# Performance work log

Hardware: AMD Instinct MI355X
Metric: run time of the kernel (lower is better)

## Reference

```python
import jax, jax.numpy as jnp
import numpy as np

ND, NL, E, M = 8000, 16000, 60000, 50000  # disease nodes, lncrna nodes, edges, label edges
H = 16  # attention heads


def _gat(h_src, h_dst, src, dst, Ws, Wd, a_s, a_d, b, n_dst):
    # PyG GATConv: bipartite, concat heads, add_self_loops=False, negative_slope=0.2
    Hh, C = a_s.shape
    zs = (h_src @ Ws).reshape(-1, Hh, C)   # [Ns,H,C]
    zd = (h_dst @ Wd).reshape(-1, Hh, C)   # [Nd,H,C]
    al = (zs * a_s).sum(-1)[src] + (zd * a_d).sum(-1)[dst]  # [E,H]
    al = jax.nn.leaky_relu(al, negative_slope=0.2)
    m = jax.ops.segment_max(al, dst, num_segments=n_dst)
    m = jnp.where(jnp.isfinite(m), m, 0.0)  # guard empty segments
    e = jnp.exp(al - m[dst])
    s = jax.ops.segment_sum(e, dst, num_segments=n_dst)
    alpha = e / (s[dst] + 1e-16)            # softmax over incoming edges per dst
    msg = zs[src] * alpha[:, :, None]       # [E,H,C]
    out = jax.ops.segment_sum(msg, dst, num_segments=n_dst)
    return out.reshape(n_dst, Hh * C) + b


def _head_mean(x):
    x = jax.nn.relu(x)
    return x.reshape(x.shape[0], H, -1).mean(axis=1)


def _forward(x_d, x_l, emb_d, emb_l, lin_dw, lin_db, lin_lw, lin_lb,
             Wsrc1, Wdst1, asrc1, adst1, b1,
             Wsrc2, Wdst2, asrc2, adst2, b2,
             Wsrc3, Wdst3, asrc3, adst3, b3,
             pw, pb, fc1w, fc1b, fc2w, fc2b,
             node_id_d, node_id_l, edge_src, edge_dst, label_src, label_dst):
    hd = x_d @ lin_dw + lin_db + emb_d[node_id_d]   # [ND,128]
    hl = x_l @ lin_lw + lin_lb + emb_l[node_id_l]   # [NL,128]
    for (Ws, Wd, a_s, a_d, b) in ((Wsrc1, Wdst1, asrc1, adst1, b1),
                                  (Wsrc2, Wdst2, asrc2, adst2, b2),
                                  (Wsrc3, Wdst3, asrc3, adst3, b3)):
        # to_hetero: edge-type 0 = disease->lncrna (target lncrna); 1 = reverse
        out_l = _gat(hd, hl, edge_src, edge_dst, Ws[0], Wd[0], a_s[0], a_d[0], b[0], NL)
        out_d = _gat(hl, hd, edge_dst, edge_src, Ws[1], Wd[1], a_s[1], a_d[1], b[1], ND)
        hd, hl = _head_mean(out_d), _head_mean(out_l)
    # penalty scaling (per node type after to_hetero); transformer branch is dead code
    hd = hd * jnp.exp(hd @ pw[0] + pb[0])
    hl = hl * jnp.exp(hl @ pw[1] + pb[1])
    f = jnp.concatenate([hd[label_src], hl[label_dst]], axis=-1)  # [M,64]
    return jax.nn.relu(f @ fc1w + fc1b) @ fc2w + fc2b              # [M,1]


def setup_inputs():
    key = jax.random.key(0)
    ks = jax.random.split(key, 40)
    def rn(i, shape, scale=1.0):
        return jax.random.normal(ks[i], shape, dtype=jnp.float32) * scale
    return dict(
        x_d=rn(0, (ND, 412)), x_l=rn(1, (NL, 240)),
        node_id_d=jnp.arange(ND), node_id_l=jnp.arange(NL),
        edge_src=jax.random.randint(ks[2], (E,), 0, ND),
        edge_dst=jax.random.randint(ks[3], (E,), 0, NL),
        label_src=jax.random.randint(ks[4], (M,), 0, ND),
        label_dst=jax.random.randint(ks[5], (M,), 0, NL),
        emb_d=rn(6, (ND, 128), 0.1), emb_l=rn(7, (NL, 128), 0.1),
        lin_dw=rn(8, (412, 128), 412 ** -0.5), lin_db=rn(9, (128,), 0.02),
        lin_lw=rn(10, (240, 128), 240 ** -0.5), lin_lb=rn(11, (128,), 0.02),
        Wsrc1=rn(12, (2, 128, 2048), 128 ** -0.5), Wdst1=rn(13, (2, 128, 2048), 128 ** -0.5),
        asrc1=rn(14, (2, H, 128), 0.05), adst1=rn(15, (2, H, 128), 0.05), b1=rn(16, (2, 2048), 0.02),
        Wsrc2=rn(17, (2, 128, 2048), 128 ** -0.5), Wdst2=rn(18, (2, 128, 2048), 128 ** -0.5),
        asrc2=rn(19, (2, H, 128), 0.05), adst2=rn(20, (2, H, 128), 0.05), b2=rn(21, (2, 2048), 0.02),
        Wsrc3=rn(22, (2, 128, 512), 128 ** -0.5), Wdst3=rn(23, (2, 128, 512), 128 ** -0.5),
        asrc3=rn(24, (2, H, 32), 0.05), adst3=rn(25, (2, H, 32), 0.05), b3=rn(26, (2, 512), 0.02),
        pw=rn(27, (2, 32, 1), 0.05), pb=rn(28, (2, 1), 0.01),
        fc1w=rn(29, (64, 64), 64 ** -0.5), fc1b=rn(30, (64,), 0.02),
        fc2w=rn(31, (64, 1), 64 ** -0.5), fc2b=rn(32, (1,), 0.02),
    )


def reference(x_d, x_l, node_id_d, node_id_l, edge_src, edge_dst, label_src, label_dst,
              emb_d, emb_l, lin_dw, lin_db, lin_lw, lin_lb,
              Wsrc1, Wdst1, asrc1, adst1, b1,
              Wsrc2, Wdst2, asrc2, adst2, b2,
              Wsrc3, Wdst3, asrc3, adst3, b3,
              pw, pb, fc1w, fc1b, fc2w, fc2b):
    return _forward(x_d, x_l, emb_d, emb_l, lin_dw, lin_db, lin_lw, lin_lb,
                    Wsrc1, Wdst1, asrc1, adst1, b1,
                    Wsrc2, Wdst2, asrc2, adst2, b2,
                    Wsrc3, Wdst3, asrc3, adst3, b3,
                    pw, pb, fc1w, fc1b, fc2w, fc2b,
                    node_id_d, node_id_l, edge_src, edge_dst, label_src, label_dst)
```

## Files before the change

kernel.cpp:

```cpp
#include <hip/hip_runtime.h>
#include <cstdint>
#include <cstddef>

#define ND 8000
#define NL 16000
#define NE 60000
#define NM 50000

#define BM 64
#define BN 64
#define BK 16

typedef __attribute__((ext_vector_type(8))) short bf16x8;
typedef __attribute__((ext_vector_type(4))) float f32x4;
typedef __attribute__((ext_vector_type(8))) unsigned int u32x8;

__device__ __forceinline__ unsigned short f2bf(float x) {
    unsigned int u = __float_as_uint(x);
    unsigned int r = (u + 0x7FFFu + ((u >> 16) & 1u)) >> 16;
    return (unsigned short)r;
}
__device__ __forceinline__ float bf2f(unsigned short b) {
    return __uint_as_float(((unsigned int)b) << 16);
}
__device__ __forceinline__ float lrelu(float x) {
    return x >= 0.f ? x : 0.2f * x;
}

__global__ __launch_bounds__(256) void gemm3_kernel(
    const float* __restrict__ hd, const float* __restrict__ hl,
    const float* __restrict__ W,
    float* __restrict__ zs3d, float* __restrict__ zs3l)
{
    __shared__ float As[BK][BM + 4];
    __shared__ float Bs[BK][BN + 4];
    int mt = blockIdx.y;
    const float* A; const float* B; float* Cm;
    if (mt < 125) { A = hd; B = W; Cm = zs3d; }
    else { mt -= 125; A = hl; B = W + 128 * 512; Cm = zs3l; }
    const int tid = threadIdx.x;
    const int tx = tid & 15, ty = tid >> 4;
    const int bm = mt * BM, bn = blockIdx.x * BN;
    float acc[4][4] = {};
    for (int k0 = 0; k0 < 128; k0 += BK) {
#pragma unroll
        for (int i = 0; i < 4; ++i) {
            int idx = tid + i * 256;
            int ml = idx >> 4, kl = idx & 15;
            As[kl][ml] = A[(size_t)(bm + ml) * 128 + k0 + kl];
        }
#pragma unroll
        for (int i = 0; i < 4; ++i) {
            int idx = tid + i * 256;
            int kl = idx >> 6, nl = idx & 63;
            Bs[kl][nl] = B[(size_t)(k0 + kl) * 512 + bn + nl];
        }
        __syncthreads();
#pragma unroll
        for (int k = 0; k < BK; ++k) {
            float4 av = *(const float4*)&As[k][ty * 4];
            float4 bv = *(const float4*)&Bs[k][tx * 4];
            float a4[4] = {av.x, av.y, av.z, av.w};
            float b4[4] = {bv.x, bv.y, bv.z, bv.w};
#pragma unroll
            for (int i = 0; i < 4; ++i)
#pragma unroll
                for (int j = 0; j < 4; ++j)
                    acc[i][j] += a4[i] * b4[j];
        }
        __syncthreads();
    }
#pragma unroll
    for (int i = 0; i < 4; ++i) {
        int gm = bm + ty * 4 + i;
        int gn0 = bn + tx * 4;
        float4 v;
        float* vp = &v.x;
#pragma unroll
        for (int j = 0; j < 4; ++j) vp[j] = acc[i][j];
        *(float4*)&Cm[(size_t)gm * 512 + gn0] = v;
    }
}

__global__ __launch_bounds__(256) void inlin_kernel(
    const float* __restrict__ x_d, const float* __restrict__ x_l,
    const float* __restrict__ wd, const float* __restrict__ wl,
    const float* __restrict__ bd, const float* __restrict__ bl,
    const float* __restrict__ embd, const float* __restrict__ embl,
    const int* __restrict__ nidd, const int* __restrict__ nidl,
    float* __restrict__ hd, float* __restrict__ hl)
{
    __shared__ float As[BK][32 + 4];
    __shared__ float Bs[BK][BN + 4];
    int mt = blockIdx.y;
    const float* A; const float* B; const float* bias; const float* emb;
    const int* nid; float* out;
    int K;
    if (mt < 250) {
        A = x_d; B = wd; bias = bd; emb = embd; nid = nidd; out = hd; K = 412;
    } else {
        mt -= 250;
        A = x_l; B = wl; bias = bl; emb = embl; nid = nidl; out = hl; K = 240;
    }
    const int tid = threadIdx.x;
    const int tx = tid & 15, ty = tid >> 4;
    const int bm = mt * 32, bn = blockIdx.x * BN;

    const int aml0 = tid >> 4, akl0 = tid & 15;
    const int aml1 = (tid + 256) >> 4, akl1 = tid & 15;
    const int bkl = tid >> 6, bnl = tid & 63;

    float pa[2], pb[4];
    {
        int gk0 = akl0, gk1 = akl1;
        pa[0] = (gk0 < K) ? A[(size_t)(bm + aml0) * K + gk0] : 0.f;
        pa[1] = (gk1 < K) ? A[(size_t)(bm + aml1) * K + gk1] : 0.f;
#pragma unroll
        for (int i = 0; i < 4; ++i) {
            int gk = bkl + i * 4;
            pb[i] = (gk < K) ? B[(size_t)gk * 128 + bn + bnl] : 0.f;
        }
    }

    float acc[2][4] = {};
    for (int k0 = 0; k0 < K; k0 += BK) {
        As[akl0][aml0] = pa[0];
        As[akl1][aml1] = pa[1];
#pragma unroll
        for (int i = 0; i < 4; ++i)
            Bs[bkl + i * 4][bnl] = pb[i];
        __syncthreads();
        int kn = k0 + BK;
        if (kn < K) {
            int gk0 = kn + akl0, gk1 = kn + akl1;
            pa[0] = (gk0 < K) ? A[(size_t)(bm + aml0) * K + gk0] : 0.f;
            pa[1] = (gk1 < K) ? A[(size_t)(bm + aml1) * K + gk1] : 0.f;
#pragma unroll
            for (int i = 0; i < 4; ++i) {
                int gk = kn + bkl + i * 4;
                pb[i] = (gk < K) ? B[(size_t)gk * 128 + bn + bnl] : 0.f;
            }
        }
#pragma unroll
        for (int k = 0; k < BK; ++k) {
            float a0 = As[k][ty * 2];
            float a1 = As[k][ty * 2 + 1];
            float4 bv = *(const float4*)&Bs[k][tx * 4];
            float b4[4] = {bv.x, bv.y, bv.z, bv.w};
#pragma unroll
            for (int j = 0; j < 4; ++j) {
                acc[0][j] += a0 * b4[j];
                acc[1][j] += a1 * b4[j];
            }
        }
        __syncthreads();
    }
#pragma unroll
    for (int i = 0; i < 2; ++i) {
        int gm = bm + ty * 2 + i;
        int gn0 = bn + tx * 4;
        const float* ep = emb + (size_t)nid[gm] * 128 + gn0;
        float4 v;
        float* vp = &v.x;
#pragma unroll
        for (int j = 0; j < 4; ++j)
            vp[j] = acc[i][j] + bias[gn0 + j] + ep[j];
        *(float4*)&out[(size_t)gm * 128 + gn0] = v;
    }
}

__global__ void wt2_kernel(const float* __restrict__ W0, const float* __restrict__ W1,
                           unsigned short* __restrict__ WtH, unsigned short* __restrict__ WtL)
{
    int gid = blockIdx.x * 256 + threadIdx.x;
    if (gid >= 2 * 2 * 128 * 2048) return;
    int l = gid >> 19;
    int rem0 = gid & 524287;
    int dir = rem0 >> 18;
    int rem = rem0 & 262143;
    int k = rem >> 11, n = rem & 2047;
    const float* W = l ? W1 : W0;
    float v = W[(size_t)dir * 262144 + (size_t)k * 2048 + n];
    unsigned short hb = f2bf(v);
    unsigned short lb = f2bf(v - bf2f(hb));
    int u = n >> 4;
    int lane = (n & 15) + 16 * ((k >> 3) & 3);
    size_t o = (size_t)l * 524288 + (size_t)dir * 262144 +
               ((size_t)u * 4 + (k >> 5)) * 512 + lane * 8 + (k & 7);
    WtH[o] = hb;
    WtL[o] = lb;
}

__global__ __launch_bounds__(256) void gemm2r_kernel(
    const unsigned int* __restrict__ haggP,
    const unsigned short* __restrict__ WtH, const unsigned short* __restrict__ WtL,
    const float* __restrict__ bias, float* __restrict__ out, int M)
{
    const int wave = threadIdx.x >> 6;
    const int lane = threadIdx.x & 63;
    const int i = blockIdx.x;
    const int cb = (i >> 3) & 3;
    const int mt = (i >> 5) * 8 + (i & 7);
    if (mt >= (M >> 6)) return;
    const int m0 = mt * 64 + wave * 16;
    const int t = m0 >> 4;
    const int row = lane & 15;
    const int quad = lane >> 4;

    f32x4 mean[2] = {};

    u32x8 pA[4];
#pragma unroll
    for (int kc = 0; kc < 4; ++kc)
        pA[kc] = *(const u32x8*)(haggP + (((size_t)t * 16 + 0) * 4 + kc) * 512 + lane * 8);

    for (int h = 0; h < 16; ++h) {
        bf16x8 aH[4], aL[4];
#pragma unroll
        for (int kc = 0; kc < 4; ++kc) {
#pragma unroll
            for (int ii = 0; ii < 8; ++ii) {
                aH[kc][ii] = (short)(pA[kc][ii] & 0xffffu);
                aL[kc][ii] = (short)(pA[kc][ii] >> 16);
            }
        }
        if (h < 15) {
#pragma unroll
            for (int kc = 0; kc < 4; ++kc)
                pA[kc] = *(const u32x8*)(haggP + (((size_t)t * 16 + h + 1) * 4 + kc) * 512 + lane * 8);
        }

        f32x4 accH[2], accL[2];
#pragma unroll
        for (int ctl = 0; ctl < 2; ++ctl) {
            float bv = bias[h * 128 + cb * 32 + ctl * 16 + row];
            accH[ctl] = (f32x4){bv, bv, bv, bv};
            accL[ctl] = (f32x4){0.f, 0.f, 0.f, 0.f};
        }
#pragma unroll
        for (int kc = 0; kc < 4; ++kc) {
#pragma unroll
            for (int ctl = 0; ctl < 2; ++ctl) {
                const int u = h * 8 + cb * 2 + ctl;
                const size_t boff = ((size_t)u * 4 + kc) * 512 + lane * 8;
                bf16x8 bH = *(const bf16x8*)(WtH + boff);
                bf16x8 bL = *(const bf16x8*)(WtL + boff);
                accH[ctl] = __builtin_amdgcn_mfma_f32_16x16x32_bf16(aH[kc], bH, accH[ctl], 0, 0, 0);
                accL[ctl] = __builtin_amdgcn_mfma_f32_16x16x32_bf16(aH[kc], bL, accL[ctl], 0, 0, 0);
                accL[ctl] = __builtin_amdgcn_mfma_f32_16x16x32_bf16(aL[kc], bH, accL[ctl], 0, 0, 0);
            }
        }
#pragma unroll
        for (int ctl = 0; ctl < 2; ++ctl)
#pragma unroll
            for (int r = 0; r < 4; ++r)
                mean[ctl][r] += fmaxf(accH[ctl][r] + accL[ctl][r], 0.f);
    }

#pragma unroll
    for (int ctl = 0; ctl < 2; ++ctl) {
        int c = cb * 32 + ctl * 16 + row;
#pragma unroll
        for (int r = 0; r < 4; ++r) {
            int gm = m0 + quad * 4 + r;
            out[(size_t)gm * 128 + c] = mean[ctl][r] * (1.f / 16.f);
        }
    }
}

__global__ void fold3_kernel(
    const float* __restrict__ Ws1, const float* __restrict__ Wd1,
    const float* __restrict__ as1, const float* __restrict__ ad1,
    const float* __restrict__ Ws2, const float* __restrict__ Wd2,
    const float* __restrict__ as2, const float* __restrict__ ad2,
    const float* __restrict__ Ws3, const float* __restrict__ Wd3,
    const float* __restrict__ as3, const float* __restrict__ ad3,
    float* __restrict__ fw3)
{
    int gid = blockIdx.x * blockDim.x + threadIdx.x;
    if (gid >= 3 * 4 * 128 * 16) return;
    int l = gid / 8192, rem1 = gid % 8192;
    int f = rem1 / 2048, rem = rem1 % 2048;
    int k = rem >> 4, h = rem & 15;
    int Ntot = (l == 2) ? 512 : 2048;
    int C = Ntot >> 4;
    const float* W;
    const float* a;
    if (l == 0) { W = (f & 1) ? Wd1 : Ws1; a = (f & 1) ? ad1 : as1; }
    else if (l == 1) { W = (f & 1) ? Wd2 : Ws2; a = (f & 1) ? ad2 : as2; }
    else { W = (f & 1) ? Wd3 : Ws3; a = (f & 1) ? ad3 : as3; }
    if (f >= 2) { W += 128 * Ntot; a += 16 * C; }
    float s = 0.f;
    for (int c = 0; c < C; ++c) s += W[(size_t)k * Ntot + h * C + c] * a[h * C + c];
    fw3[gid] = s;
}

__global__ __launch_bounds__(256) void score2both_kernel(
    const float* __restrict__ Hd, const float* __restrict__ Hl,
    const float* __restrict__ fw,
    float* __restrict__ ssb0, float* __restrict__ sdb1,
    float* __restrict__ sdb0, float* __restrict__ ssb1)
{
    __shared__ float hs[16 * 128];
    __shared__ float wa[128 * 16];
    __shared__ float wb[128 * 16];
    int b = blockIdx.x;
    const float* Hf; const float* WfA; const float* WfB;
    float* outA; float* outB; int n0;
    if (b < ND / 16) {
        Hf = Hd; WfA = fw; WfB = fw + 3 * 2048; outA = ssb0; outB = sdb1; n0 = b * 16;
    } else {
        Hf = Hl; WfA = fw + 1 * 2048; WfB = fw + 2 * 2048; outA = sdb0; outB = ssb1;
        n0 = (b - ND / 16) * 16;
    }
    int tid = threadIdx.x;
#pragma unroll
    for (int i = 0; i < 8; ++i) {
        int idx = tid + i * 256;
        int nl = idx >> 7, k = idx & 127;
        hs[idx] = Hf[(size_t)(n0 + nl) * 128 + k];
        wa[idx] = WfA[idx];
        wb[idx] = WfB[idx];
    }
    __syncthreads();
    int nl = tid >> 4, h = tid & 15;
    float sa = 0.f, sb = 0.f;
    for (int k = 0; k < 128; ++k) {
        float hv = hs[nl * 128 + k];
        sa += hv * wa[k * 16 + h];
        sb += hv * wb[k * 16 + h];
    }
    int gn = n0 + nl;
    outA[gn * 16 + h] = sa;
    outB[gn * 16 + h] = sb;
}

__global__ void ms_kernel(
    const int* __restrict__ esrc, const int* __restrict__ edst,
    const float* __restrict__ ssb0, const float* __restrict__ sdb0,
    const float* __restrict__ ssb1, const float* __restrict__ sdb1,
    const int* __restrict__ offl, const int* __restrict__ csrl, float* __restrict__ msl,
    const int* __restrict__ offd, const int* __restrict__ csrd, float* __restrict__ msd)
{
    int t = blockIdx.x * 256 + threadIdx.x;
    const int* off; const int* csr; const int* srcidx;
    const float* ss; float sdv; float* ms; int d, h;
    if (t < NL * 16) {
        d = t >> 4; h = t & 15;
        off = offl; csr = csrl; srcidx = esrc; ss = ssb0;
        sdv = sdb0[d * 16 + h]; ms = msl;
    } else {
        t -= NL * 16;
        if (t >= ND * 16) return;
        d = t >> 4; h = t & 15;
        off = offd; csr = csrd; srcidx = edst; ss = ssb1;
        sdv = sdb1[d * 16 + h]; ms = msd;
    }
    int e0 = off[d], e1 = off[d + 1];
    float m = -1e30f, s = 0.f;
    for (int e = e0; e < e1; ++e) {
        int sn = srcidx[csr[e]];
        float a = lrelu(ss[sn * 16 + h] + sdv);
        if (a > m) { s = s * __expf(m - a) + 1.f; m = a; }
        else s += __expf(a - m);
    }
    ms[d * 32 + h] = m;
    ms[d * 32 + 16 + h] = s + 1e-16f;
}

__global__ void hist_kernel(const int* __restrict__ esrc, const int* __restrict__ edst,
                            int* __restrict__ degl, int* __restrict__ degd)
{
    int e = blockIdx.x * blockDim.x + threadIdx.x;
    if (e >= NE) return;
    atomicAdd(&degl[edst[e]], 1);
    atomicAdd(&degd[esrc[e]], 1);
}

__global__ __launch_bounds__(1024) void scan2_kernel(
    const int* __restrict__ degA, int* __restrict__ offA, int nA,
    const int* __restrict__ degB, int* __restrict__ offB, int nB)
{
    __shared__ int ps[1024];
    const int* deg = blockIdx.x ? degB : degA;
    int* off = blockIdx.x ? offB : offA;
    int n = blockIdx.x ? nB : nA;
    int tid = threadIdx.x;
    int chunk = (n + 1023) >> 10;
    int start = tid * chunk, end = min(start + chunk, n);
    int p = 0;
    for (int i = start; i < end; ++i) p += deg[i];
    ps[tid] = p;
    __syncthreads();
    for (int o = 1; o < 1024; o <<= 1) {
        int v = (tid >= o) ? ps[tid - o] : 0;
        __syncthreads();
        ps[tid] += v;
        __syncthreads();
    }
    int run = ps[tid] - p;
    for (int i = start; i < end; ++i) { off[i] = run; run += deg[i]; }
    if (tid == 1023) off[n] = ps[1023];
}

__global__ void scatter_kernel(const int* __restrict__ esrc, const int* __restrict__ edst,
                               const int* __restrict__ offl, const int* __restrict__ offd,
                               int* __restrict__ curl, int* __restrict__ curd,
                               int* __restrict__ csrl, int* __restrict__ csrd)
{
    int e = blockIdx.x * blockDim.x + threadIdx.x;
    if (e >= NE) return;
    int dl = edst[e]; int p = atomicAdd(&curl[dl], 1); csrl[offl[dl] + p] = e;
    int dd = esrc[e]; int q = atomicAdd(&curd[dd], 1); csrd[offd[dd] + q] = e;
}

__global__ __launch_bounds__(256) void hagg_kernel(
    const float* __restrict__ hsrc,
    const float* __restrict__ ss,
    const float* __restrict__ sd,
    const float* __restrict__ ms,
    const int* __restrict__ off, const int* __restrict__ csr, const int* __restrict__ srcidx,
    unsigned int* __restrict__ haggP)
{
    __shared__ float alpha_s[2][8][17];
    __shared__ int src_s[2][8];
    const int d0 = blockIdx.x * 2;
    const int tid = threadIdx.x;

    const int half = tid >> 7;
    const int c = tid & 127;
    const int d = d0 + half;
    const int my_e0 = off[d];
    const int my_deg = off[d + 1] - my_e0;
    const int deg0 = off[d0 + 1] - off[d0];
    const int deg1 = off[d0 + 2] - off[d0 + 1];
    const int degmax = deg0 > deg1 ? deg0 : deg1;
    const int ntrip = (degmax + 7) >> 3;

    float acc[16];
#pragma unroll
    for (int h = 0; h < 16; ++h) acc[h] = 0.f;

    for (int trip = 0; trip < ntrip; ++trip) {
        int ce = trip * 8;
        {
            int ei = c >> 4, h = c & 15;
            if (ce + ei < my_deg) {
                int eid = csr[my_e0 + ce + ei];
                int sn = srcidx[eid];
                float a = lrelu(ss[sn * 16 + h] + sd[d * 16 + h]);
                alpha_s[half][ei][h] = __expf(a - ms[d * 32 + h]) / ms[d * 32 + 16 + h];
                if (h == 0) src_s[half][ei] = sn;
            }
        }
        __syncthreads();
        int nc = min(8, my_deg - ce);
        for (int ei = 0; ei < nc; ++ei) {
            float v = hsrc[(size_t)src_s[half][ei] * 128 + c];
#pragma unroll
            for (int h = 0; h < 16; ++h)
                acc[h] += alpha_s[half][ei][h] * v;
        }
        __syncthreads();
    }

    const int t = d >> 4;
    const int lane8 = ((d & 15) + 16 * ((c >> 3) & 3)) * 8 + (c & 7);
    const int kc = c >> 5;
#pragma unroll
    for (int h = 0; h < 16; ++h) {
        float v = acc[h];
        unsigned short hb = f2bf(v);
        unsigned short lb = f2bf(v - bf2f(hb));
        size_t idx = (((size_t)t * 16 + h) * 4 + kc) * 512 + lane8;
        haggP[idx] = (unsigned int)hb | ((unsigned int)lb << 16);
    }
}

__global__ __launch_bounds__(256) void agg32both_kernel(
    const float* __restrict__ zs3d, const float* __restrict__ zs3l,
    const float* __restrict__ ssb0, const float* __restrict__ sdb0, const float* __restrict__ msl,
    const float* __restrict__ ssb1, const float* __restrict__ sdb1, const float* __restrict__ msd,
    const int* __restrict__ offl, const int* __restrict__ csrl,
    const int* __restrict__ offd, const int* __restrict__ csrd,
    const int* __restrict__ esrc, const int* __restrict__ edst,
    const float* __restrict__ bias512,
    const float* __restrict__ pw, const float* __restrict__ pb,
    float* __restrict__ hlp, float* __restrict__ hdp)
{
    __shared__ float alpha_s[16][17];
    __shared__ int src_s[16];
    __shared__ float lds_out[512];
    __shared__ float hrow[32];
    int d = blockIdx.x;
    const float* zs; const float* ss; const float* sd; const float* ms;
    const int* off; const int* csr; const int* srcidx;
    const float* bias; const float* pwt; const float* pbt; float* out;
    if (d < NL) {
        zs = zs3d; ss = ssb0; sd = sdb0; ms = msl;
        off = offl; csr = csrl; srcidx = esrc;
        bias = bias512; pwt = pw + 32; pbt = pb + 1; out = hlp;
    } else {
        d -= NL;
        zs = zs3l; ss = ssb1; sd = sdb1; ms = msd;
        off = offd; csr = csrd; srcidx = edst;
        bias = bias512 + 512; pwt = pw; pbt = pb; out = hdp;
    }
    const int tid = threadIdx.x;
    const int e0 = off[d], e1 = off[d + 1];

    float acc0 = 0.f, acc1 = 0.f;
    const int hsel = tid >> 4;

    for (int ce = e0; ce < e1; ce += 16) {
        int nc = min(16, e1 - ce);
        if (tid < nc * 16) {
            int ei = tid >> 4, h = tid & 15;
            int eid = csr[ce + ei];
            int sn = srcidx[eid];
            float a = lrelu(ss[sn * 16 + h] + sd[d * 16 + h]);
            alpha_s[ei][h] = __expf(a - ms[d * 32 + h]) / ms[d * 32 + 16 + h];
            if (h == 0) src_s[ei] = sn;
        }
        __syncthreads();
        for (int ei = 0; ei < nc; ++ei) {
            float a = alpha_s[ei][hsel];
            float2 v = *(const float2*)(zs + (size_t)src_s[ei] * 512 + tid * 2);
            acc0 += a * v.x;
            acc1 += a * v.y;
        }
        __syncthreads();
    }

    lds_out[tid * 2] = fmaxf(acc0 + bias[tid * 2], 0.f);
    lds_out[tid * 2 + 1] = fmaxf(acc1 + bias[tid * 2 + 1], 0.f);
    __syncthreads();
    if (tid < 32) {
        float s = 0.f;
#pragma unroll
        for (int hh = 0; hh < 16; ++hh) s += lds_out[hh * 32 + tid];
        hrow[tid] = s * (1.f / 16.f);
    }
    __syncthreads();
    if (tid < 32) {
        float t = pbt[0];
#pragma unroll
        for (int c = 0; c < 32; ++c) t += hrow[c] * pwt[c];
        out[(size_t)d * 32 + tid] = hrow[tid] * expf(t);
    }
}

__global__ __launch_bounds__(256) void mlp_kernel(
    const float* __restrict__ hd, const float* __restrict__ hl,
    const int* __restrict__ ls, const int* __restrict__ ld,
    const float* __restrict__ w1, const float* __restrict__ b1,
    const float* __restrict__ w2, const float* __restrict__ b2,
    float* __restrict__ out, int M)
{
    __shared__ float w1s[64 * 64];
    __shared__ float b1s[64];
    __shared__ float w2s[64];
    int tid = threadIdx.x;
#pragma unroll
    for (int i = 0; i < 16; ++i) w1s[tid + i * 256] = w1[tid + i * 256];
    if (tid < 64) { b1s[tid] = b1[tid]; w2s[tid] = w2[tid]; }
    __syncthreads();
    int m = blockIdx.x * 256 + tid;
    if (m >= M) return;
    float f[64];
    const float* hp = hd + (size_t)ls[m] * 32;
    const float* lp = hl + (size_t)ld[m] * 32;
#pragma unroll
    for (int c = 0; c < 32; ++c) { f[c] = hp[c]; f[32 + c] = lp[c]; }
    float o = b2[0];
    for (int j = 0; j < 64; ++j) {
        float hj = b1s[j];
#pragma unroll
        for (int k = 0; k < 64; ++k) hj += f[k] * w1s[k * 64 + j];
        hj = fmaxf(hj, 0.f);
        o += hj * w2s[j];
    }
    out[m] = o;
}

extern "C" void kernel_launch(void* const* d_in, const int* in_sizes, int n_in,
                              void* d_out, int out_size, void* d_ws, size_t ws_size,
                              hipStream_t stream)
{
    const float* x_d = (const float*)d_in[0];
    const float* x_l = (const float*)d_in[1];
    const int* node_id_d = (const int*)d_in[2];
    const int* node_id_l = (const int*)d_in[3];
    const int* edge_src = (const int*)d_in[4];
    const int* edge_dst = (const int*)d_in[5];
    const int* label_src = (const int*)d_in[6];
    const int* label_dst = (const int*)d_in[7];
    const float* emb_d = (const float*)d_in[8];
    const float* emb_l = (const float*)d_in[9];
    const float* lin_dw = (const float*)d_in[10];
    const float* lin_db = (const float*)d_in[11];
    const float* lin_lw = (const float*)d_in[12];
    const float* lin_lb = (const float*)d_in[13];
    const float* Ws[3] = {(const float*)d_in[14], (const float*)d_in[19], (const float*)d_in[24]};
    const float* Wd[3] = {(const float*)d_in[15], (const float*)d_in[20], (const float*)d_in[25]};
    const float* as_[3] = {(const float*)d_in[16], (const float*)d_in[21], (const float*)d_in[26]};
    const float* ad_[3] = {(const float*)d_in[17], (const float*)d_in[22], (const float*)d_in[27]};
    const float* bb[3] = {(const float*)d_in[18], (const float*)d_in[23], (const float*)d_in[28]};
    const float* pw = (const float*)d_in[29];
    const float* pb = (const float*)d_in[30];
    const float* fc1w = (const float*)d_in[31];
    const float* fc1b = (const float*)d_in[32];
    const float* fc2w = (const float*)d_in[33];
    const float* fc2b = (const float*)d_in[34];

    char* wsb = (char*)d_ws;
    size_t woff = 0;
    auto carve = [&](size_t bytes) -> void* {
        woff = (woff + 255) & ~(size_t)255;
        void* p = wsb + woff;
        woff += bytes;
        return p;
    };
    float* hdA = (float*)carve((size_t)ND * 128 * 4);
    float* hlA = (float*)carve((size_t)NL * 128 * 4);
    float* hdB = (float*)carve((size_t)ND * 128 * 4);
    float* hlB = (float*)carve((size_t)NL * 128 * 4);
    unsigned int* haggP = (unsigned int*)carve((size_t)NL * 2048 * 4);
    unsigned short* WtH = (unsigned short*)carve((size_t)2 * 2 * 2048 * 128 * 2);
    unsigned short* WtL = (unsigned short*)carve((size_t)2 * 2 * 2048 * 128 * 2);
    float* ssb0 = (float*)carve((size_t)ND * 16 * 4);
    float* sdb0 = (float*)carve((size_t)NL * 16 * 4);
    float* ssb1 = (float*)carve((size_t)NL * 16 * 4);
    float* sdb1 = (float*)carve((size_t)ND * 16 * 4);
    float* msl = (float*)carve((size_t)NL * 32 * 4);
    float* msd = (float*)carve((size_t)ND * 32 * 4);
    float* fw3 = (float*)carve((size_t)3 * 4 * 2048 * 4);
    int* degl = (int*)carve((size_t)(2 * (NL + ND)) * 4);
    int* degd = degl + NL;
    int* curl = degd + ND;
    int* curd = curl + NL;
    int* offl = (int*)carve((size_t)(NL + 1) * 4);
    int* offd = (int*)carve((size_t)(ND + 1) * 4);
    int* csrl = (int*)carve((size_t)NE * 4);
    int* csrd = (int*)carve((size_t)NE * 4);
    float* hdp = (float*)carve((size_t)ND * 32 * 4);
    float* hlp = (float*)carve((size_t)NL * 32 * 4);

    hipMemsetAsync(degl, 0, (size_t)2 * (NL + ND) * 4, stream);

    hist_kernel<<<(NE + 255) / 256, 256, 0, stream>>>(edge_src, edge_dst, degl, degd);
    scan2_kernel<<<2, 1024, 0, stream>>>(degl, offl, NL, degd, offd, ND);
    scatter_kernel<<<(NE + 255) / 256, 256, 0, stream>>>(edge_src, edge_dst, offl, offd, curl, curd, csrl, csrd);

    fold3_kernel<<<(3 * 8192 + 255) / 256, 256, 0, stream>>>(
        Ws[0], Wd[0], as_[0], ad_[0], Ws[1], Wd[1], as_[1], ad_[1],
        Ws[2], Wd[2], as_[2], ad_[2], fw3);
    wt2_kernel<<<(2 * 524288 + 255) / 256, 256, 0, stream>>>(Ws[0], Ws[1], WtH, WtL);

    inlin_kernel<<<dim3(2, 750), 256, 0, stream>>>(
        x_d, x_l, lin_dw, lin_lw, lin_db, lin_lb, emb_d, emb_l,
        node_id_d, node_id_l, hdA, hlA);

    float* hd_cur = hdA; float* hd_nxt = hdB;
    float* hl_cur = hlA; float* hl_nxt = hlB;

    const int grid_ms = ((NL + ND) * 16 + 255) / 256;
    const int gridNL = ((NL / 64 + 7) / 8) * 32;
    const int gridND = ((ND / 64 + 7) / 8) * 32;

    for (int L = 0; L < 2; ++L) {
        const float* fw = fw3 + (size_t)L * 8192;
        const unsigned short* wtH = WtH + (size_t)L * 524288;
        const unsigned short* wtL = WtL + (size_t)L * 524288;

        score2both_kernel<<<ND / 16 + NL / 16, 256, 0, stream>>>(
            hd_cur, hl_cur, fw, ssb0, sdb1, sdb0, ssb1);
        ms_kernel<<<grid_ms, 256, 0, stream>>>(edge_src, edge_dst, ssb0, sdb0, ssb1, sdb1,
                                               offl, csrl, msl, offd, csrd, msd);

        hagg_kernel<<<NL / 2, 256, 0, stream>>>(hd_cur, ssb0, sdb0, msl, offl, csrl, edge_src, haggP);
        gemm2r_kernel<<<gridNL, 256, 0, stream>>>(haggP, wtH, wtL, bb[L], hl_nxt, NL);

        hagg_kernel<<<ND / 2, 256, 0, stream>>>(hl_cur, ssb1, sdb1, msd, offd, csrd, edge_dst, haggP);
        gemm2r_kernel<<<gridND, 256, 0, stream>>>(haggP,
                                                  wtH + (size_t)2048 * 128, wtL + (size_t)2048 * 128,
                                                  bb[L] + 2048, hd_nxt, ND);

        float* t;
        t = hd_cur; hd_cur = hd_nxt; hd_nxt = t;
        t = hl_cur; hl_cur = hl_nxt; hl_nxt = t;
    }

    {
        const float* fw = fw3 + 2 * 8192;
        float* zs3d = (float*)haggP;
        float* zs3l = (float*)haggP + (size_t)ND * 512;
        score2both_kernel<<<ND / 16 + NL / 16, 256, 0, stream>>>(
            hd_cur, hl_cur, fw, ssb0, sdb1, sdb0, ssb1);
        ms_kernel<<<grid_ms, 256, 0, stream>>>(edge_src, edge_dst, ssb0, sdb0, ssb1, sdb1,
                                               offl, csrl, msl, offd, csrd, msd);

        gemm3_kernel<<<dim3(512 / BN, 125 + 250), 256, 0, stream>>>(
            hd_cur, hl_cur, Ws[2], zs3d, zs3l);

        agg32both_kernel<<<NL + ND, 256, 0, stream>>>(
            zs3d, zs3l, ssb0, sdb0, msl, ssb1, sdb1, msd,
            offl, csrl, offd, csrd, edge_src, edge_dst,
            bb[2], pw, pb, hlp, hdp);
    }

    mlp_kernel<<<(NM + 255) / 256, 256, 0, stream>>>(hdp, hlp, label_src, label_dst,
                                                     fc1w, fc1b, fc2w, fc2b, (float*)d_out, NM);
}
```

Measured before the change: 775.5 us.

## Stage gemm2r weight tiles in double-buffered LDS via global_load_lds, widen column block

```diff
diff --git a/kernel.cpp b/kernel.cpp
--- a/kernel.cpp
+++ b/kernel.cpp
@@ -25,6 +25,12 @@
 }
 __device__ __forceinline__ float lrelu(float x) {
     return x >= 0.f ? x : 0.2f * x;
+}
+
+__device__ __forceinline__ void gl_lds16(const void* g, void* l) {
+    __builtin_amdgcn_global_load_lds(
+        (const __attribute__((address_space(1))) void*)g,
+        (__attribute__((address_space(3))) void*)l, 16, 0, 0);
 }
 
 __global__ __launch_bounds__(256) void gemm3_kernel(
@@ -196,24 +202,39 @@
     const unsigned short* __restrict__ WtH, const unsigned short* __restrict__ WtL,
     const float* __restrict__ bias, float* __restrict__ out, int M)
 {
-    const int wave = threadIdx.x >> 6;
-    const int lane = threadIdx.x & 63;
+    __shared__ unsigned short BsH[2][8192];
+    __shared__ unsigned short BsL[2][8192];
+
+    const int tid = threadIdx.x;
+    const int wave = tid >> 6;
+    const int lane = tid & 63;
     const int i = blockIdx.x;
-    const int cb = (i >> 3) & 3;
-    const int mt = (i >> 5) * 8 + (i & 7);
-    if (mt >= (M >> 6)) return;
+    const int cb = i & 1;
+    const int mt = i >> 1;
     const int m0 = mt * 64 + wave * 16;
     const int t = m0 >> 4;
     const int row = lane & 15;
     const int quad = lane >> 4;
 
-    f32x4 mean[2] = {};
+    const unsigned short* gHb = WtH + (size_t)cb * 8192;
+    const unsigned short* gLb = WtL + (size_t)cb * 8192;
 
     u32x8 pA[4];
+
+    f32x4 mean[4] = {};
+
+#pragma unroll
+    for (int j = 0; j < 4; ++j) {
+        int o = (tid + j * 256) * 16;
+        gl_lds16((const char*)gHb + o, (char*)&BsH[0][0] + o);
+        gl_lds16((const char*)gLb + o, (char*)&BsL[0][0] + o);
+    }
 #pragma unroll
     for (int kc = 0; kc < 4; ++kc)
         pA[kc] = *(const u32x8*)(haggP + (((size_t)t * 16 + 0) * 4 + kc) * 512 + lane * 8);
-
+    __syncthreads();
+
+    int buf = 0;
     for (int h = 0; h < 16; ++h) {
         bf16x8 aH[4], aL[4];
 #pragma unroll
@@ -225,41 +246,45 @@
             }
         }
         if (h < 15) {
+            const char* gH = (const char*)(gHb + (size_t)(h + 1) * 16384);
+            const char* gL = (const char*)(gLb + (size_t)(h + 1) * 16384);
+            char* lH = (char*)&BsH[buf ^ 1][0];
+            char* lL = (char*)&BsL[buf ^ 1][0];
+#pragma unroll
+            for (int j = 0; j < 4; ++j) {
+                int o = (tid + j * 256) * 16;
+                gl_lds16(gH + o, lH + o);
+                gl_lds16(gL + o, lL + o);
+            }
 #pragma unroll
             for (int kc = 0; kc < 4; ++kc)
                 pA[kc] = *(const u32x8*)(haggP + (((size_t)t * 16 + h + 1) * 4 + kc) * 512 + lane * 8);
         }
 
-        f32x4 accH[2], accL[2];
-#pragma unroll
-        for (int ctl = 0; ctl < 2; ++ctl) {
-            float bv = bias[h * 128 + cb * 32 + ctl * 16 + row];
-            accH[ctl] = (f32x4){bv, bv, bv, bv};
-            accL[ctl] = (f32x4){0.f, 0.f, 0.f, 0.f};
-        }
-#pragma unroll
-        for (int kc = 0; kc < 4; ++kc) {
-#pragma unroll
-            for (int ctl = 0; ctl < 2; ++ctl) {
-                const int u = h * 8 + cb * 2 + ctl;
-                const size_t boff = ((size_t)u * 4 + kc) * 512 + lane * 8;
-                bf16x8 bH = *(const bf16x8*)(WtH + boff);
-                bf16x8 bL = *(const bf16x8*)(WtL + boff);
-                accH[ctl] = __builtin_amdgcn_mfma_f32_16x16x32_bf16(aH[kc], bH, accH[ctl], 0, 0, 0);
-                accL[ctl] = __builtin_amdgcn_mfma_f32_16x16x32_bf16(aH[kc], bL, accL[ctl], 0, 0, 0);
-                accL[ctl] = __builtin_amdgcn_mfma_f32_16x16x32_bf16(aL[kc], bH, accL[ctl], 0, 0, 0);
+#pragma unroll
+        for (int ctl = 0; ctl < 4; ++ctl) {
+            float bv = bias[h * 128 + cb * 64 + ctl * 16 + row];
+            f32x4 accH = (f32x4){bv, bv, bv, bv};
+            f32x4 accL = (f32x4){0.f, 0.f, 0.f, 0.f};
+#pragma unroll
+            for (int kc = 0; kc < 4; ++kc) {
+                bf16x8 bH = *(const bf16x8*)&BsH[buf][(ctl * 4 + kc) * 512 + lane * 8];
+                bf16x8 bL = *(const bf16x8*)&BsL[buf][(ctl * 4 + kc) * 512 + lane * 8];
+                accH = __builtin_amdgcn_mfma_f32_16x16x32_bf16(aH[kc], bH, accH, 0, 0, 0);
+                accL = __builtin_amdgcn_mfma_f32_16x16x32_bf16(aH[kc], bL, accL, 0, 0, 0);
+                accL = __builtin_amdgcn_mfma_f32_16x16x32_bf16(aL[kc], bH, accL, 0, 0, 0);
             }
-        }
-#pragma unroll
-        for (int ctl = 0; ctl < 2; ++ctl)
 #pragma unroll
             for (int r = 0; r < 4; ++r)
-                mean[ctl][r] += fmaxf(accH[ctl][r] + accL[ctl][r], 0.f);
-    }
-
-#pragma unroll
-    for (int ctl = 0; ctl < 2; ++ctl) {
-        int c = cb * 32 + ctl * 16 + row;
+                mean[ctl][r] += fmaxf(accH[r] + accL[r], 0.f);
+        }
+        __syncthreads();
+        buf ^= 1;
+    }
+
+#pragma unroll
+    for (int ctl = 0; ctl < 4; ++ctl) {
+        int c = cb * 64 + ctl * 16 + row;
 #pragma unroll
         for (int r = 0; r < 4; ++r) {
             int gm = m0 + quad * 4 + r;
@@ -665,8 +690,8 @@
     float* hl_cur = hlA; float* hl_nxt = hlB;
 
     const int grid_ms = ((NL + ND) * 16 + 255) / 256;
-    const int gridNL = ((NL / 64 + 7) / 8) * 32;
-    const int gridND = ((ND / 64 + 7) / 8) * 32;
+    const int gridNL = (NL / 64) * 2;
+    const int gridND = (ND / 64) * 2;
 
     for (int L = 0; L < 2; ++L) {
         const float* fw = fw3 + (size_t)L * 8192;
```

After: 711.2 us. 8.3% less time.
